# Performance work log

Measured on AMD Instinct MI355X. Metric: run time of the kernel, lower is better.

Reference implementation:

```python
import jax, jax.numpy as jnp
import numpy as np

DIM = 1024
NUM_ATT = 8
NUM_HEADS = 16
HEAD_DIM = DIM // NUM_HEADS
ROPE_BASE = 10000.0
NEG_INF = -1e9


def _rope(x):
    # x: [B, H, L, hd]; torchtune-style interleaved RoPE applied along the sequence axis.
    B, H, L, hd = x.shape
    pos = jnp.arange(L, dtype=jnp.float32)
    inv_freq = 1.0 / (ROPE_BASE ** (jnp.arange(0, hd, 2, dtype=jnp.float32) / hd))
    ang = pos[:, None] * inv_freq[None, :]          # [L, hd/2]
    cos = jnp.cos(ang)[None, None]                  # [1,1,L,hd/2]
    sin = jnp.sin(ang)[None, None]
    xr = x.reshape(B, H, L, hd // 2, 2)
    x0, x1 = xr[..., 0], xr[..., 1]
    out = jnp.stack([x0 * cos - x1 * sin, x1 * cos + x0 * sin], axis=-1)
    return out.reshape(B, H, L, hd).astype(x.dtype)


def setup_inputs() -> dict:
    key = jax.random.key(0)
    ks = jax.random.split(key, 7)
    B, L = 32, 512
    x = jax.random.normal(ks[0], (B, L, DIM), dtype=jnp.float32)
    s = 0.02  # init scale for numerical sanity (init choice, not math)
    query_projs = jax.random.normal(ks[1], (NUM_ATT, DIM, DIM), dtype=jnp.float32) * s
    key_projs = jax.random.normal(ks[2], (NUM_ATT, DIM, DIM), dtype=jnp.float32) * s
    value_projs = jax.random.normal(ks[3], (NUM_ATT, DIM, DIM), dtype=jnp.float32) * s
    out_projs = jax.random.normal(ks[4], (NUM_ATT, DIM, DIM), dtype=jnp.float32) * s
    router_w = jax.random.normal(ks[5], (DIM, NUM_ATT), dtype=jnp.float32) * s
    router_b = jnp.zeros((NUM_ATT,), dtype=jnp.float32)
    return {"x": x, "query_projs": query_projs, "key_projs": key_projs,
            "value_projs": value_projs, "out_projs": out_projs,
            "router_w": router_w, "router_b": router_b}


def reference(x, query_projs, key_projs, value_projs, out_projs, router_w, router_b):
    B, L, D = x.shape
    H, hd = NUM_HEADS, HEAD_DIM
    scale = hd ** -0.5

    # top-1 routing on mean-pooled tokens
    logits = x.mean(axis=1) @ router_w + router_b       # [B, E]
    attn_probs = jax.nn.softmax(logits, axis=-1)
    routes = jnp.argmax(attn_probs, axis=-1)            # [B] int

    # per-batch weight gather (the memory-bound irregular access) + bmm
    qw = query_projs[routes]                             # [B, D, D]
    kw = key_projs[routes]
    vw = value_projs[routes]
    q = jnp.einsum('bld,bde->ble', x, qw)
    k = jnp.einsum('bld,bde->ble', x, kw)
    v = jnp.einsum('bld,bde->ble', x, vw)

    q = q.reshape(B, L, H, hd).transpose(0, 2, 1, 3)     # [B,H,L,hd]
    k = k.reshape(B, L, H, hd).transpose(0, 2, 1, 3)
    v = v.reshape(B, L, H, hd).transpose(0, 2, 1, 3)

    q = _rope(q)
    k = _rope(k)

    scores = jnp.einsum('bhld,bhmd->bhlm', q, k) * scale  # [B,H,L,L]
    causal = jnp.triu(jnp.ones((L, L), dtype=bool), k=1)  # True above diag = masked
    scores = jnp.where(causal[None, None], NEG_INF, scores)
    attn = jax.nn.softmax(scores, axis=-1)
    out = jnp.einsum('bhlm,bhmd->bhld', attn, v)          # [B,H,L,hd]
    out = out.transpose(0, 2, 1, 3).reshape(B, L, D)

    ow = out_projs[routes]                                # [B, D, D]
    out = jnp.einsum('bld,bde->ble', out, ow)
    return out, attn_probs
```

## Files before the change

kernel.cpp:

```cpp
#include <hip/hip_runtime.h>


typedef __attribute__((ext_vector_type(8))) short bf16x8;
typedef __attribute__((ext_vector_type(4))) float f32x4;

typedef const __attribute__((address_space(1))) unsigned short* gas_t;
typedef __attribute__((address_space(3))) unsigned short* las_t;

#define OFF_PART   (0ull)
#define OFF_ROUTES (2ull << 20)
#define OFF_XB     (3ull << 20)
#define OFF_WT     (40ull << 20)
#define OFF_QKV    (112ull << 20)

__device__ __forceinline__ unsigned short f2bf(float f){
  unsigned int u = __float_as_uint(f);
  u += 0x7fffu + ((u >> 16) & 1u);
  return (unsigned short)(u >> 16);
}


__global__ void meanpool_kernel(const float* __restrict__ x, float* __restrict__ part,
                                unsigned short* __restrict__ xb){
  const int b = blockIdx.x, lc = blockIdx.y, t = threadIdx.x;
  const size_t base = ((size_t)b*512 + lc*32)*1024;
  const float* xs = x + base;
  unsigned short* xo = xb + base;
  float4 a = {0.f, 0.f, 0.f, 0.f};
  for (int l = 0; l < 32; ++l){
    const float4 v = *(const float4*)(xs + l*1024 + t*4);
    a.x += v.x; a.y += v.y; a.z += v.z; a.w += v.w;
    ushort4 pk;
    pk.x = f2bf(v.x); pk.y = f2bf(v.y); pk.z = f2bf(v.z); pk.w = f2bf(v.w);
    *(ushort4*)(xo + l*1024 + t*4) = pk;
  }
  *(float4*)(part + ((size_t)b*16 + lc)*1024 + t*4) = a;
}


__global__ void router_kernel(const float* __restrict__ part,
                              const float* __restrict__ rw,
                              const float* __restrict__ rbias,
                              float* __restrict__ probs,
                              int* __restrict__ routes){
  const int b = blockIdx.x, t = threadIdx.x;
  const int lane = t & 63, wave = t >> 6;
  __shared__ float wred[4][8];
  float p[8] = {0.f,0.f,0.f,0.f,0.f,0.f,0.f,0.f};
  #pragma unroll
  for (int k = 0; k < 4; ++k){
    const int d = t + k*256;
    float s = 0.f;
    #pragma unroll
    for (int lc = 0; lc < 16; ++lc)
      s += part[((size_t)b*16 + lc)*1024 + d];
    s *= (1.0f/512.0f);
    const float4 w0 = *(const float4*)(rw + d*8);
    const float4 w1 = *(const float4*)(rw + d*8 + 4);
    p[0] = fmaf(s, w0.x, p[0]); p[1] = fmaf(s, w0.y, p[1]);
    p[2] = fmaf(s, w0.z, p[2]); p[3] = fmaf(s, w0.w, p[3]);
    p[4] = fmaf(s, w1.x, p[4]); p[5] = fmaf(s, w1.y, p[5]);
    p[6] = fmaf(s, w1.z, p[6]); p[7] = fmaf(s, w1.w, p[7]);
  }
  #pragma unroll
  for (int off = 1; off < 64; off <<= 1)
    #pragma unroll
    for (int e = 0; e < 8; ++e)
      p[e] += __shfl_xor(p[e], off, 64);
  if (lane == 0){
    #pragma unroll
    for (int e = 0; e < 8; ++e) wred[wave][e] = p[e];
  }
  __syncthreads();
  if (t == 0){
    float lg[8], mx = -3e38f; int am = 0;
    #pragma unroll
    for (int e = 0; e < 8; ++e){
      lg[e] = wred[0][e] + wred[1][e] + wred[2][e] + wred[3][e] + rbias[e];
      if (lg[e] > mx){ mx = lg[e]; am = e; }
    }
    float sum = 0.f, ex[8];
    #pragma unroll
    for (int e = 0; e < 8; ++e){ ex[e] = __expf(lg[e] - mx); sum += ex[e]; }
    const float inv = 1.0f / sum;
    #pragma unroll
    for (int e = 0; e < 8; ++e) probs[b*8 + e] = ex[e] * inv;
    routes[b] = am;
  }
}


__global__ void wcast_kernel(const float* __restrict__ W, unsigned short* __restrict__ Wt){
  __shared__ float tile[64][65];
  const int mtx = blockIdx.z;
  const float* Wm = W + (size_t)mtx*1024*1024;
  unsigned short* Wo = Wt + (size_t)mtx*1024*1024;
  const int t = threadIdx.x;
  const int r = t >> 4;
  const int c4 = t & 15;
  const int gx = blockIdx.x*64, gy = blockIdx.y*64;
  #pragma unroll
  for (int k = 0; k < 4; ++k){
    const int rr = r + 16*k;
    const float4 v = *(const float4*)(Wm + (size_t)(gy + rr)*1024 + gx + c4*4);
    tile[rr][c4*4+0] = v.x; tile[rr][c4*4+1] = v.y;
    tile[rr][c4*4+2] = v.z; tile[rr][c4*4+3] = v.w;
  }
  __syncthreads();
  #pragma unroll
  for (int k = 0; k < 4; ++k){
    const int rr = r + 16*k;
    ushort4 pk;
    pk.x = f2bf(tile[c4*4+0][rr]); pk.y = f2bf(tile[c4*4+1][rr]);
    pk.z = f2bf(tile[c4*4+2][rr]); pk.w = f2bf(tile[c4*4+3][rr]);
    *(ushort4*)(Wo + (size_t)(gx + rr)*1024 + gy + c4*4) = pk;
  }
}


template<int MODE>
__global__ __launch_bounds__(512, 2) void gemm_kernel(
    const unsigned short* __restrict__ A,
    const unsigned short* __restrict__ Wt,
    const int* __restrict__ routes,
    unsigned short* __restrict__ qkvout,
    float* __restrict__ outf)
{
  __shared__ __align__(16) unsigned short As[2][256*64];
  __shared__ __align__(16) unsigned short Bs[2][256*64];

  const int f = blockIdx.x + blockIdx.y*8;
  const int CH = (MODE == 0) ? 96 : 32;
  const int wg = (f & 7)*CH + (f >> 3);
  const int slice = wg >> 3;
  const int tile  = wg & 7;
  const int m0 = (tile >> 2)*256;
  const int n0 = (tile & 3)*256;
  const int b = (MODE == 0) ? (slice/3) : slice;
  const int p = (MODE == 0) ? (slice - b*3) : 0;

  const int route = routes[b];
  const unsigned short* Ab = A + (size_t)b*512*1024;
  const unsigned short* Wb = Wt + (size_t)((MODE == 0) ? (p*8 + route) : route)*1024*1024;

  const int t = threadIdx.x;
  const int lane = t & 63;
  const int wave = t >> 6;
  const int wm = (wave >> 2)*128;
  const int wn = (wave & 3)*64;
  const int quad = lane >> 4;
  const int ln = lane & 15;

  const int srow = t >> 3;
  const int schA = (t & 7) ^ (srow & 7);
  const int schB = (t & 7) ^ ((t >> 5) & 7);
  const unsigned short* gA0 = Ab + (size_t)(m0 + srow)*1024 + schA*8;
  const unsigned short* gB0 = Wb + (size_t)(n0 + srow)*1024 + schB*8;

  const int w8 = ln & 7;
  const int aO0 = (wm + ln)*64 + ((quad    ) ^ w8)*8;
  const int aO1 = (wm + ln)*64 + ((quad + 4) ^ w8)*8;
  const int bO0 = (wn + ln*4)*64 + ((quad    ) ^ w8)*8;
  const int bO1 = (wn + ln*4)*64 + ((quad + 4) ^ w8)*8;

  f32x4 acc[8][4] = {};
  bf16x8 a0[4][2], a1[4][2], b01[2][2], b23[2][2];

#define STAGE(c_, T_) do { \
    const size_t ko_ = (size_t)(T_)*64; \
    las_t dA_ = (las_t)(&As[c_][0]) + (size_t)t*8; \
    las_t dB_ = (las_t)(&Bs[c_][0]) + (size_t)t*8; \
    _Pragma("unroll") \
    for (int k_ = 0; k_ < 4; ++k_){ \
      __builtin_amdgcn_global_load_lds((gas_t)(gA0 + ko_ + (size_t)k_*65536), dA_ + k_*4096, 16, 0, 0); \
      __builtin_amdgcn_global_load_lds((gas_t)(gB0 + ko_ + (size_t)k_*65536), dB_ + k_*4096, 16, 0, 0); \
    } \
  } while (0)

#define RD(ptr_, off_) (*(const bf16x8*)((ptr_) + (off_)))
#define READ_F0(pA_, pB_) do { \
    _Pragma("unroll") for (int f_ = 0; f_ < 4; ++f_){ \
      a0[f_][0] = RD(pA_, aO0 + f_*1024); a0[f_][1] = RD(pA_, aO1 + f_*1024); } \
    _Pragma("unroll") for (int f_ = 0; f_ < 2; ++f_){ \
      b01[f_][0] = RD(pB_, bO0 + f_*64); b01[f_][1] = RD(pB_, bO1 + f_*64); } \
  } while (0)
#define READ_F1(pA_) do { \
    _Pragma("unroll") for (int f_ = 0; f_ < 4; ++f_){ \
      a1[f_][0] = RD(pA_, aO0 + (4+f_)*1024); a1[f_][1] = RD(pA_, aO1 + (4+f_)*1024); } \
  } while (0)
#define READ_F2(pB_) do { \
    _Pragma("unroll") for (int f_ = 0; f_ < 2; ++f_){ \
      b23[f_][0] = RD(pB_, bO0 + (2+f_)*64); b23[f_][1] = RD(pB_, bO1 + (2+f_)*64); } \
  } while (0)

#define MSET(AF_, BF_, IB_, JB_) do { \
    _Pragma("unroll") for (int f_ = 0; f_ < 4; ++f_) \
    _Pragma("unroll") for (int n_ = 0; n_ < 2; ++n_) \
    _Pragma("unroll") for (int k_ = 0; k_ < 2; ++k_) \
      acc[IB_+f_][JB_+n_] = __builtin_amdgcn_mfma_f32_16x16x32_bf16( \
          AF_[f_][k_], BF_[n_][k_], acc[IB_+f_][JB_+n_], 0, 0, 0); \
  } while (0)

  STAGE(0, 0);
  STAGE(1, 1);
  asm volatile("s_waitcnt vmcnt(8)" ::: "memory");
  __builtin_amdgcn_s_barrier();
  READ_F0((&As[0][0]), (&Bs[0][0]));

  for (int g = 0; g < 16; ++g){
    const int c = g & 1;
    const unsigned short* pA  = &As[c][0];
    const unsigned short* pB  = &Bs[c][0];
    const unsigned short* pAn = &As[c ^ 1][0];
    const unsigned short* pBn = &Bs[c ^ 1][0];

    READ_F1(pA);
    __builtin_amdgcn_s_barrier();
    asm volatile("s_waitcnt lgkmcnt(8)" ::: "memory");
    __builtin_amdgcn_sched_barrier(0);
    __builtin_amdgcn_s_setprio(1);
    MSET(a0, b01, 0, 0);
    __builtin_amdgcn_s_setprio(0);
    __builtin_amdgcn_s_barrier();

    READ_F2(pB);
    __builtin_amdgcn_s_barrier();
    asm volatile("s_waitcnt lgkmcnt(4)" ::: "memory");
    __builtin_amdgcn_sched_barrier(0);
    __builtin_amdgcn_s_setprio(1);
    MSET(a1, b01, 4, 0);
    __builtin_amdgcn_s_setprio(0);
    __builtin_amdgcn_s_barrier();

    asm volatile("s_waitcnt lgkmcnt(0)" ::: "memory");
    __builtin_amdgcn_sched_barrier(0);
    __builtin_amdgcn_s_setprio(1);
    MSET(a1, b23, 4, 2);
    __builtin_amdgcn_s_setprio(0);
    __builtin_amdgcn_s_barrier();

    if (g < 14){
      STAGE(c, g + 2);
      asm volatile("s_waitcnt vmcnt(8)" ::: "memory");
    } else if (g == 14){
      asm volatile("s_waitcnt vmcnt(0)" ::: "memory");
    }
    __builtin_amdgcn_s_barrier();
    __builtin_amdgcn_s_setprio(1);
    MSET(a0, b23, 0, 2);
    __builtin_amdgcn_s_setprio(0);
    if (g < 15) READ_F0(pAn, pBn);
    __builtin_amdgcn_s_barrier();
  }
#undef STAGE
#undef RD
#undef READ_F0
#undef READ_F1
#undef READ_F2
#undef MSET

  if (MODE == 0){
    const size_t PSZ = (size_t)32*16*512*64;
    const int h = (n0 + wn) >> 6;
    if (p < 2){
      const int eh0 = ln*4;
      const float invf0 = exp2f(-0.41524101f * (float)(ln*2));
      const float invf1 = invf0 * 0.74989420832f;
      float sc0, cc0, sc1, cc1;
      __sincosf(invf0, &sc0, &cc0);
      __sincosf(invf1, &sc1, &cc1);
      unsigned short* outp = qkvout + ((((size_t)p*32 + b)*16 + h)*512)*64 + eh0;
      #pragma unroll
      for (int fm = 0; fm < 8; ++fm){
        const int l0 = m0 + wm + fm*16 + quad*4;
        float s0, c0, s1, c1;
        __sincosf((float)l0 * invf0, &s0, &c0);
        __sincosf((float)l0 * invf1, &s1, &c1);
        #pragma unroll
        for (int r = 0; r < 4; ++r){
          const int l = l0 + r;
          const float x0 = acc[fm][0][r], x1 = acc[fm][1][r];
          const float x2 = acc[fm][2][r], x3 = acc[fm][3][r];
          ushort4 pk;
          pk.x = f2bf(x0*c0 - x1*s0);
          pk.y = f2bf(x1*c0 + x0*s0);
          pk.z = f2bf(x2*c1 - x3*s1);
          pk.w = f2bf(x3*c1 + x2*s1);
          *(ushort4*)(outp + (size_t)l*64) = pk;
          const float nc0 = c0*cc0 - s0*sc0, ns0 = s0*cc0 + c0*sc0;
          const float nc1 = c1*cc1 - s1*sc1, ns1 = s1*cc1 + c1*sc1;
          c0 = nc0; s0 = ns0; c1 = nc1; s1 = ns1;
        }
      }
    } else {
      #pragma unroll
      for (int fn = 0; fn < 4; ++fn){
        const int eh = ln*4 + fn;
        unsigned short* outp = qkvout + 2*PSZ + (((size_t)b*16 + h)*64 + eh)*512;
        #pragma unroll
        for (int fm = 0; fm < 8; ++fm){
          const int l0 = m0 + wm + fm*16 + quad*4;
          ushort4 pk;
          pk.x = f2bf(acc[fm][fn][0]); pk.y = f2bf(acc[fm][fn][1]);
          pk.z = f2bf(acc[fm][fn][2]); pk.w = f2bf(acc[fm][fn][3]);
          *(ushort4*)(outp + l0) = pk;
        }
      }
    }
  } else {
    const int e0 = n0 + wn + ln*4;
    #pragma unroll
    for (int fm = 0; fm < 8; ++fm){
      #pragma unroll
      for (int r = 0; r < 4; ++r){
        const int l = m0 + wm + fm*16 + quad*4 + r;
        float4 f4;
        f4.x = acc[fm][0][r]; f4.y = acc[fm][1][r];
        f4.z = acc[fm][2][r]; f4.w = acc[fm][3][r];
        *(float4*)(outf + ((size_t)b*512 + l)*1024 + e0) = f4;
      }
    }
  }
}


#define PSTR 72

__global__ __launch_bounds__(256, 3) void attn_kernel(
    const unsigned short* __restrict__ qkv,
    unsigned short* __restrict__ ctx)
{
  __shared__ __align__(16) unsigned short Ks[2][64*64];
  __shared__ __align__(16) unsigned short Vts[2][64*64];
  __shared__ __align__(16) unsigned short Ps[4][32*PSTR];

  int wg = blockIdx.x + (blockIdx.y << 2) + (blockIdx.z << 6);
  wg = (wg & 7) * 256 + (wg >> 3);
  const int b  = wg >> 6;
  const int h  = (wg >> 2) & 15;
  const int qt = wg & 3;

  const size_t HO  = (((size_t)b)*16 + h)*512*64;
  const size_t PSZ = (size_t)32*16*512*64;
  const unsigned short* Qg  = qkv + HO;
  const unsigned short* Kg  = qkv + PSZ + HO;
  const unsigned short* Vtg = qkv + 2*PSZ + HO;

  const int t    = threadIdx.x;
  const int lane = t & 63;
  const int wave = t >> 6;
  const int quad = lane >> 4;
  const int ln   = lane & 15;

  const int u0 = t, u1 = t + 256;
  const int kr0 = u0 >> 3, kc0 = (u0 & 7) ^ (kr0 & 7);
  const int kr1 = u1 >> 3, kc1 = (u1 & 7) ^ (kr1 & 7);

  bf16x8 aq[2][2];
  #pragma unroll
  for (int rg = 0; rg < 2; ++rg){
    const int row = qt*128 + rg*64 + wave*16 + ln;
    #pragma unroll
    for (int ks = 0; ks < 2; ++ks)
      aq[rg][ks] = *(const bf16x8*)(Qg + (size_t)row*64 + ks*32 + quad*8);
  }

  const int ktEnd = 2*qt + 1;

  __builtin_amdgcn_global_load_lds((gas_t)(Kg  + kr0*64  + kc0*8), (las_t)(Ks[0]  + u0*8), 16,0,0);
  __builtin_amdgcn_global_load_lds((gas_t)(Kg  + kr1*64  + kc1*8), (las_t)(Ks[0]  + u1*8), 16,0,0);
  __builtin_amdgcn_global_load_lds((gas_t)(Vtg + kr0*512 + kc0*8), (las_t)(Vts[0] + u0*8), 16,0,0);
  __builtin_amdgcn_global_load_lds((gas_t)(Vtg + kr1*512 + kc1*8), (las_t)(Vts[0] + u1*8), 16,0,0);

  float m_r[2][4], l_r[2][4];
  #pragma unroll
  for (int rg = 0; rg < 2; ++rg)
    #pragma unroll
    for (int r = 0; r < 4; ++r){ m_r[rg][r] = -3e38f; l_r[rg][r] = 0.f; }
  f32x4 o[2][4] = {};

  const int swzl = ln & 7;
  unsigned short* Pw = Ps[wave];
  const int rowoff = wave*16 + quad*4;

  for (int kt = 0; kt <= ktEnd; ++kt){
    __syncthreads();
    if (kt < ktEnd){
      const unsigned short* Kn  = Kg + (kt+1)*4096;
      const int col = (kt+1)*64;
      unsigned short* kb = Ks[(kt+1)&1];
      unsigned short* vb = Vts[(kt+1)&1];
      __builtin_amdgcn_global_load_lds((gas_t)(Kn  + kr0*64 + kc0*8),        (las_t)(kb + u0*8), 16,0,0);
      __builtin_amdgcn_global_load_lds((gas_t)(Kn  + kr1*64 + kc1*8),        (las_t)(kb + u1*8), 16,0,0);
      __builtin_amdgcn_global_load_lds((gas_t)(Vtg + kr0*512 + col + kc0*8), (las_t)(vb + u0*8), 16,0,0);
      __builtin_amdgcn_global_load_lds((gas_t)(Vtg + kr1*512 + col + kc1*8), (las_t)(vb + u1*8), 16,0,0);
    }
    const unsigned short* ks_ = Ks[kt&1];
    const unsigned short* vt_ = Vts[kt&1];

    #pragma unroll
    for (int rg = 0; rg < 2; ++rg){
      if (rg == 0 && kt > 2*qt) continue;
      const bool diag = (kt == 2*qt + rg);

      f32x4 s[4] = {};
      __builtin_amdgcn_s_setprio(1);
      #pragma unroll
      for (int ks2 = 0; ks2 < 2; ++ks2){
        #pragma unroll
        for (int kn = 0; kn < 4; ++kn){
          const bf16x8 bk = *(const bf16x8*)(ks_ + (kn*16+ln)*64 + (((quad + ks2*4) ^ swzl))*8);
          s[kn] = __builtin_amdgcn_mfma_f32_16x16x32_bf16(aq[rg][ks2], bk, s[kn], 0, 0, 0);
        }
      }
      __builtin_amdgcn_s_setprio(0);

      float p[4][4], lm[4] = {-3e38f,-3e38f,-3e38f,-3e38f};
      #pragma unroll
      for (int kn = 0; kn < 4; ++kn){
        const int col = kn*16 + ln;
        #pragma unroll
        for (int r = 0; r < 4; ++r){
          float v = s[kn][r] * 0.125f;
          if (diag && col > rowoff + r) v = -1e9f;
          p[kn][r] = v;
          lm[r] = fmaxf(lm[r], v);
        }
      }
      #pragma unroll
      for (int off = 1; off < 16; off <<= 1)
        #pragma unroll
        for (int r = 0; r < 4; ++r)
          lm[r] = fmaxf(lm[r], __shfl_xor(lm[r], off, 64));
      float alpha[4], rsum[4];
      #pragma unroll
      for (int r = 0; r < 4; ++r){
        const float mn = fmaxf(m_r[rg][r], lm[r]);
        alpha[r] = __expf(m_r[rg][r] - mn);
        m_r[rg][r] = mn;
      }
      #pragma unroll
      for (int kn = 0; kn < 4; ++kn)
        #pragma unroll
        for (int r = 0; r < 4; ++r)
          p[kn][r] = __expf(p[kn][r] - m_r[rg][r]);
      #pragma unroll
      for (int r = 0; r < 4; ++r)
        rsum[r] = (p[0][r] + p[1][r]) + (p[2][r] + p[3][r]);
      #pragma unroll
      for (int off = 1; off < 16; off <<= 1)
        #pragma unroll
        for (int r = 0; r < 4; ++r)
          rsum[r] += __shfl_xor(rsum[r], off, 64);
      #pragma unroll
      for (int r = 0; r < 4; ++r) l_r[rg][r] = l_r[rg][r]*alpha[r] + rsum[r];
      #pragma unroll
      for (int dn = 0; dn < 4; ++dn)
        #pragma unroll
        for (int r = 0; r < 4; ++r)
          o[rg][dn][r] *= alpha[r];

      #pragma unroll
      for (int kn = 0; kn < 4; ++kn)
        #pragma unroll
        for (int r = 0; r < 4; ++r)
          Pw[(rg*16 + quad*4 + r)*PSTR + kn*16 + ln] = f2bf(p[kn][r]);

      __builtin_amdgcn_s_setprio(1);
      #pragma unroll
      for (int ks2 = 0; ks2 < 2; ++ks2){
        const bf16x8 ap = *(const bf16x8*)(Pw + (rg*16 + ln)*PSTR + quad*8 + ks2*32);
        #pragma unroll
        for (int dn = 0; dn < 4; ++dn){
          const bf16x8 bv = *(const bf16x8*)(vt_ + (dn*16+ln)*64 + (((quad + ks2*4) ^ swzl))*8);
          o[rg][dn] = __builtin_amdgcn_mfma_f32_16x16x32_bf16(ap, bv, o[rg][dn], 0, 0, 0);
        }
      }
      __builtin_amdgcn_s_setprio(0);
    }
  }

  #pragma unroll
  for (int rg = 0; rg < 2; ++rg){
    #pragma unroll
    for (int r = 0; r < 4; ++r){
      const float inv = 1.0f / l_r[rg][r];
      const int row = qt*128 + rg*64 + wave*16 + quad*4 + r;
      unsigned short* op = ctx + ((size_t)b*512 + row)*1024 + h*64 + ln;
      #pragma unroll
      for (int dn = 0; dn < 4; ++dn)
        op[dn*16] = f2bf(o[rg][dn][r] * inv);
    }
  }
}


extern "C" void kernel_launch(void* const* d_in, const int* in_sizes, int n_in,
                              void* d_out, int out_size, void* d_ws, size_t ws_size,
                              hipStream_t stream) {
  const float* x     = (const float*)d_in[0];
  const float* qw    = (const float*)d_in[1];
  const float* kw    = (const float*)d_in[2];
  const float* vw    = (const float*)d_in[3];
  const float* ow    = (const float*)d_in[4];
  const float* rw    = (const float*)d_in[5];
  const float* rbias = (const float*)d_in[6];
  float* out = (float*)d_out;
  char* ws = (char*)d_ws;

  float* part            = (float*)(ws + OFF_PART);
  int* routes            = (int*)(ws + OFF_ROUTES);
  unsigned short* xb     = (unsigned short*)(ws + OFF_XB);
  unsigned short* wt     = (unsigned short*)(ws + OFF_WT);
  unsigned short* qkvbuf = (unsigned short*)(ws + OFF_QKV);
  unsigned short* ctx    = xb;
  float* probs = out + (size_t)32*512*1024;

  meanpool_kernel<<<dim3(32, 16), 256, 0, stream>>>(x, part, xb);
  router_kernel<<<32, 256, 0, stream>>>(part, rw, rbias, probs, routes);
  wcast_kernel<<<dim3(16, 16, 8), 256, 0, stream>>>(qw, wt);
  wcast_kernel<<<dim3(16, 16, 8), 256, 0, stream>>>(kw, wt + (size_t)8*1024*1024);
  wcast_kernel<<<dim3(16, 16, 8), 256, 0, stream>>>(vw, wt + (size_t)16*1024*1024);
  wcast_kernel<<<dim3(16, 16, 8), 256, 0, stream>>>(ow, wt + (size_t)24*1024*1024);
  gemm_kernel<0><<<dim3(8, 96), 512, 0, stream>>>(xb, wt, routes, qkvbuf, nullptr);
  attn_kernel<<<dim3(4, 16, 32), 256, 0, stream>>>(qkvbuf, ctx);
  gemm_kernel<1><<<dim3(8, 32), 512, 0, stream>>>(ctx, wt + (size_t)24*1024*1024, routes,
                                                  nullptr, out);
}
```

Baseline: 509.9 us.

## Merge weight casts into one launch, split QKV GEMM per projection, drop attention swizzle

The four weight-cast launches become a single launch that selects the source matrix by blockIdx.z. The fused QKV GEMM launch (96 slices) is split into three separate launches, one per projection, each taking the projection index as a kernel argument. The attention kernel's workgroup index remapping (an XCD-aware swizzle) is removed in favour of direct block indices. Launch overhead moves in opposite directions (fewer cast launches, more GEMM launches), and losing the swizzle may hurt L2 locality across chiplets.

Measured after the change: 509.8 us. Within noise of the previous version (-0.0%).

```diff
diff --git a/kernel.cpp b/kernel.cpp
--- a/kernel.cpp
+++ b/kernel.cpp
@@ -90,11 +90,13 @@
 }
 
 
-__global__ void wcast_kernel(const float* __restrict__ W, unsigned short* __restrict__ Wt){
+__global__ void wcast_kernel(const float* __restrict__ qw, const float* __restrict__ kw,
+                             const float* __restrict__ vw, const float* __restrict__ ow,
+                             unsigned short* __restrict__ Wt){
   __shared__ float tile[64][65];
-  const int mtx = blockIdx.z;
-  const float* Wm = W + (size_t)mtx*1024*1024;
-  unsigned short* Wo = Wt + (size_t)mtx*1024*1024;
+  const int z = blockIdx.z;
+  const float* Wm = (z < 8 ? qw : z < 16 ? kw : z < 24 ? vw : ow) + (size_t)(z & 7)*1024*1024;
+  unsigned short* Wo = Wt + (size_t)z*1024*1024;
   const int t = threadIdx.x;
   const int r = t >> 4;
   const int c4 = t & 15;
@@ -124,24 +126,22 @@
     const unsigned short* __restrict__ Wt,
     const int* __restrict__ routes,
     unsigned short* __restrict__ qkvout,
-    float* __restrict__ outf)
+    float* __restrict__ outf,
+    int pp)
 {
   __shared__ __align__(16) unsigned short As[2][256*64];
   __shared__ __align__(16) unsigned short Bs[2][256*64];
 
   const int f = blockIdx.x + blockIdx.y*8;
-  const int CH = (MODE == 0) ? 96 : 32;
-  const int wg = (f & 7)*CH + (f >> 3);
-  const int slice = wg >> 3;
-  const int tile  = wg & 7;
+  const int wg = (f & 7)*32 + (f >> 3);
+  const int b    = wg >> 3;
+  const int tile = wg & 7;
   const int m0 = (tile >> 2)*256;
   const int n0 = (tile & 3)*256;
-  const int b = (MODE == 0) ? (slice/3) : slice;
-  const int p = (MODE == 0) ? (slice - b*3) : 0;
 
   const int route = routes[b];
   const unsigned short* Ab = A + (size_t)b*512*1024;
-  const unsigned short* Wb = Wt + (size_t)((MODE == 0) ? (p*8 + route) : route)*1024*1024;
+  const unsigned short* Wb = Wt + (size_t)((MODE == 0) ? (pp*8 + route) : route)*1024*1024;
 
   const int t = threadIdx.x;
   const int lane = t & 63;
@@ -262,14 +262,14 @@
   if (MODE == 0){
     const size_t PSZ = (size_t)32*16*512*64;
     const int h = (n0 + wn) >> 6;
-    if (p < 2){
+    if (pp < 2){
       const int eh0 = ln*4;
       const float invf0 = exp2f(-0.41524101f * (float)(ln*2));
       const float invf1 = invf0 * 0.74989420832f;
       float sc0, cc0, sc1, cc1;
       __sincosf(invf0, &sc0, &cc0);
       __sincosf(invf1, &sc1, &cc1);
-      unsigned short* outp = qkvout + ((((size_t)p*32 + b)*16 + h)*512)*64 + eh0;
+      unsigned short* outp = qkvout + ((((size_t)pp*32 + b)*16 + h)*512)*64 + eh0;
       #pragma unroll
       for (int fm = 0; fm < 8; ++fm){
         const int l0 = m0 + wm + fm*16 + quad*4;
@@ -334,11 +334,7 @@
   __shared__ __align__(16) unsigned short Vts[2][64*64];
   __shared__ __align__(16) unsigned short Ps[4][32*PSTR];
 
-  int wg = blockIdx.x + (blockIdx.y << 2) + (blockIdx.z << 6);
-  wg = (wg & 7) * 256 + (wg >> 3);
-  const int b  = wg >> 6;
-  const int h  = (wg >> 2) & 15;
-  const int qt = wg & 3;
+  const int qt = blockIdx.x, h = blockIdx.y, b = blockIdx.z;
 
   const size_t HO  = (((size_t)b)*16 + h)*512*64;
   const size_t PSZ = (size_t)32*16*512*64;
@@ -518,12 +514,11 @@
 
   meanpool_kernel<<<dim3(32, 16), 256, 0, stream>>>(x, part, xb);
   router_kernel<<<32, 256, 0, stream>>>(part, rw, rbias, probs, routes);
-  wcast_kernel<<<dim3(16, 16, 8), 256, 0, stream>>>(qw, wt);
-  wcast_kernel<<<dim3(16, 16, 8), 256, 0, stream>>>(kw, wt + (size_t)8*1024*1024);
-  wcast_kernel<<<dim3(16, 16, 8), 256, 0, stream>>>(vw, wt + (size_t)16*1024*1024);
-  wcast_kernel<<<dim3(16, 16, 8), 256, 0, stream>>>(ow, wt + (size_t)24*1024*1024);
-  gemm_kernel<0><<<dim3(8, 96), 512, 0, stream>>>(xb, wt, routes, qkvbuf, nullptr);
+  wcast_kernel<<<dim3(16, 16, 32), 256, 0, stream>>>(qw, kw, vw, ow, wt);
+  gemm_kernel<0><<<dim3(8, 32), 512, 0, stream>>>(xb, wt, routes, qkvbuf, nullptr, 0);
+  gemm_kernel<0><<<dim3(8, 32), 512, 0, stream>>>(xb, wt, routes, qkvbuf, nullptr, 1);
+  gemm_kernel<0><<<dim3(8, 32), 512, 0, stream>>>(xb, wt, routes, qkvbuf, nullptr, 2);
   attn_kernel<<<dim3(4, 16, 32), 256, 0, stream>>>(qkvbuf, ctx);
   gemm_kernel<1><<<dim3(8, 32), 512, 0, stream>>>(ctx, wt + (size_t)24*1024*1024, routes,
-                                                  nullptr, out);
-}
+                                                  nullptr, out, 0);
+}
```
